# Optimization experiments

Hardware: AMD Instinct MI355X
Metric: run time of the kernel (lower is better)

The kernel has to match this reference:

```python
import jax, jax.numpy as jnp
import numpy as np

NN = 262144        # total nodes = 4096 graphs * 64 nodes
EN = 524288        # directed edges
IN_DIM = 32
H = 128
PROP_STEPS = 3


def setup_inputs() -> dict:
    key = jax.random.key(0)
    ks = jax.random.split(key, 16)
    s = lambda d: 1.0 / np.sqrt(d)
    x = jax.random.normal(ks[0], (NN, IN_DIM), dtype=jnp.float32)
    # edges: random within each 64-node graph block would be most faithful; random
    # over NN is the same access pattern workload-wise. Use per-graph-local edges.
    src = jax.random.randint(ks[1], (EN,), 0, NN, dtype=jnp.int64)
    dst = jax.random.randint(ks[2], (EN,), 0, NN, dtype=jnp.int64)
    edge_index = jnp.stack([src, dst], axis=0)
    return {
        "x": x,
        "edge_index": edge_index,
        "W_in": jax.random.normal(ks[3], (IN_DIM, H), jnp.float32) * s(IN_DIM),
        "b_in": jnp.zeros((H,), jnp.float32),
        "W_e1": jax.random.normal(ks[4], (H, H), jnp.float32) * s(H),
        "b_e1": jnp.zeros((H,), jnp.float32),
        "W_e2": jax.random.normal(ks[5], (H, H), jnp.float32) * s(H),
        "b_e2": jnp.zeros((H,), jnp.float32),
        "W_ih": jax.random.normal(ks[6], (H, 3 * H), jnp.float32) * s(H),
        "b_ih": jnp.zeros((3 * H,), jnp.float32),
        "W_hh": jax.random.normal(ks[7], (H, 3 * H), jnp.float32) * s(H),
        "b_hh": jnp.zeros((3 * H,), jnp.float32),
        "W_out": jax.random.normal(ks[8], (H, 1), jnp.float32) * s(H),
        "b_out": jnp.zeros((1,), jnp.float32),
    }


def reference(x, edge_index, W_in, b_in, W_e1, b_e1, W_e2, b_e2,
              W_ih, b_ih, W_hh, b_hh, W_out, b_out):
    in_node, out_node = edge_index[0], edge_index[1]
    nn = x.shape[0]
    # input MLP: Linear + tanh
    h = jnp.tanh(x @ W_in + b_in)                         # [NN, H]
    for _ in range(PROP_STEPS):
        # unified edge MLP (hidden tanh + linear out), applied per node then gathered
        m = jnp.tanh(h @ W_e1 + b_e1) @ W_e2 + b_e2       # [NN, H]
        msg = m[in_node]                                  # [EN, H] gather
        ssum = jax.ops.segment_sum(msg, out_node, num_segments=nn)
        cnt = jax.ops.segment_sum(jnp.ones((msg.shape[0],), msg.dtype),
                                  out_node, num_segments=nn)
        m_agg = ssum / jnp.maximum(cnt, 1.0)[:, None]     # scatter_mean, [NN, H]
        # GRU cell update: input = m_agg, hidden = h (torch GRUCell math)
        gi = m_agg @ W_ih + b_ih                          # [NN, 3H]
        gh = h @ W_hh + b_hh                              # [NN, 3H]
        i_r, i_z, i_n = jnp.split(gi, 3, axis=-1)
        h_r, h_z, h_n = jnp.split(gh, 3, axis=-1)
        r = jax.nn.sigmoid(i_r + h_r)
        z = jax.nn.sigmoid(i_z + h_z)
        n = jnp.tanh(i_n + r * h_n)
        h = (1.0 - z) * n + z * h
    # unified output head: single Linear
    return h @ W_out + b_out                              # [NN, 1]
```

## Files before the change

### kernel.cpp

```cpp
#include <hip/hip_runtime.h>

#define NN 262144
#define EN 524288
#define HD 128
#define IND 32

#define NT64  (NN/64)
#define GRID_E 768
#define NJOB  (NT64*2)
#define GRID_G2 512

typedef __attribute__((ext_vector_type(8))) short s16x8;
typedef __attribute__((ext_vector_type(4))) float f32x4;
typedef unsigned short u16;
typedef unsigned int u32;

#define MFMA(a,b,c) __builtin_amdgcn_mfma_f32_16x16x32_bf16(a,b,c,0,0,0)
#define SWZ(p) ((p) ^ ((((p)>>8)&7)<<4))

typedef __attribute__((address_space(1))) void gas_void;
typedef __attribute__((address_space(3))) void las_void;
__device__ __forceinline__ void gload16(const void* g, void* l){
  __builtin_amdgcn_global_load_lds((gas_void*)g, (las_void*)l, 16, 0, 0);
}

__device__ __forceinline__ u16 f2b(float f){
  u32 u = __builtin_bit_cast(u32, f);
  u = (u + 0x7fffu + ((u >> 16) & 1u)) >> 16;
  return (u16)u;
}
__device__ __forceinline__ u32 cvtpk(float lo, float hi){
  return (u32)f2b(lo) | ((u32)f2b(hi) << 16);
}
__device__ __forceinline__ float b2f(u32 lo16){ return __builtin_bit_cast(float, lo16 << 16); }
__device__ __forceinline__ float rcpf_(float x){ return __builtin_amdgcn_rcpf(x); }
__device__ __forceinline__ float exp2_(float x){ return __builtin_amdgcn_exp2f(x); }
__device__ __forceinline__ float fsig(float x){ return rcpf_(1.f + exp2_(x * -1.442695041f)); }
__device__ __forceinline__ float ftanh(float x){ return fmaf(-2.f, rcpf_(1.f + exp2_(x * 2.885390082f)), 1.f); }

__global__ __launch_bounds__(256) void k_w2bt(const float* __restrict__ W, u16* __restrict__ Wt, int K, int N){
  int idx = blockIdx.x*256 + threadIdx.x;
  if (idx >= K*N) return;
  int n = idx / K, k = idx - n*K;
  Wt[idx] = f2b(W[k*N + n]);
}

__global__ void k_eflag(const int* __restrict__ ei, int* __restrict__ flag){
  int v = ei[threadIdx.x*2 + 1];
  unsigned long long b = __ballot(v != 0);
  if (threadIdx.x == 0) flag[0] = (b == 0ULL) ? 1 : 0;
}
__device__ __forceinline__ int eget(const int* ei, int f, int which, int e){
  return f ? ei[(which*EN + e)*2] : ei[which*EN + e];
}

__global__ __launch_bounds__(256) void k_count(const int* __restrict__ ei, const int* __restrict__ flag, int* __restrict__ cnt){
  int e = blockIdx.x*256 + threadIdx.x;
  if (e < EN) atomicAdd(&cnt[eget(ei, flag[0], 1, e)], 1);
}
__global__ __launch_bounds__(256) void k_scan1(const int* __restrict__ cnt, int* __restrict__ excl, int* __restrict__ bsum){
  __shared__ int ws[4];
  int i = blockIdx.x*256 + threadIdx.x;
  int v = cnt[i];
  int ln = threadIdx.x & 63;
  int x = v;
  #pragma unroll
  for (int d=1; d<64; d<<=1){ int y = __shfl_up(x, d); if (ln >= d) x += y; }
  if (ln == 63) ws[threadIdx.x>>6] = x;
  __syncthreads();
  int wpre = 0;
  for (int j=0; j<(threadIdx.x>>6); ++j) wpre += ws[j];
  excl[i] = wpre + x - v;
  if (threadIdx.x == 255) bsum[blockIdx.x] = wpre + x;
}
__global__ __launch_bounds__(1024) void k_scan2(int* __restrict__ bsum){
  __shared__ int ws[16];
  int i = threadIdx.x;
  int v = bsum[i];
  int ln = i & 63;
  int x = v;
  #pragma unroll
  for (int d=1; d<64; d<<=1){ int y = __shfl_up(x, d); if (ln >= d) x += y; }
  if (ln == 63) ws[i>>6] = x;
  __syncthreads();
  int wpre = 0;
  for (int j=0; j<(i>>6); ++j) wpre += ws[j];
  bsum[i] = wpre + x - v;
}
__global__ __launch_bounds__(256) void k_scan3(const int* __restrict__ excl, const int* __restrict__ bsum, int* __restrict__ rp, int* __restrict__ cur){
  int i = blockIdx.x*256 + threadIdx.x;
  int v = excl[i] + bsum[blockIdx.x];
  rp[i] = v; cur[i] = v;
  if (i == 0) rp[NN] = EN;
}
__global__ __launch_bounds__(256) void k_fill(const int* __restrict__ ei, const int* __restrict__ flag, int* __restrict__ cur, int* __restrict__ cx){
  int e = blockIdx.x*256 + threadIdx.x;
  if (e >= EN) return;
  int f = flag[0];
  int p = atomicAdd(&cur[eget(ei, f, 1, e)], 1);
  cx[p] = eget(ei, f, 0, e);
}

__global__ __launch_bounds__(256) void k_input(const float* __restrict__ x, const u16* __restrict__ wt, const float* __restrict__ bias, u16* __restrict__ h){
  const int wv = threadIdx.x >> 6, ln = threadIdx.x & 63;
  const int l15 = ln & 15, lg = ln >> 4;
  const int base = blockIdx.x*128 + wv*32;
  s16x8 a[2];
  #pragma unroll
  for (int rt=0; rt<2; ++rt){
    const float* xp = x + (base + rt*16 + l15)*IND + lg*8;
    float4 v0 = *reinterpret_cast<const float4*>(xp);
    float4 v1 = *reinterpret_cast<const float4*>(xp + 4);
    s16x8 t;
    t[0]=(short)f2b(v0.x); t[1]=(short)f2b(v0.y); t[2]=(short)f2b(v0.z); t[3]=(short)f2b(v0.w);
    t[4]=(short)f2b(v1.x); t[5]=(short)f2b(v1.y); t[6]=(short)f2b(v1.z); t[7]=(short)f2b(v1.w);
    a[rt] = t;
  }
  #pragma unroll
  for (int cg=0; cg<8; ++cg){
    const int col = cg*16 + l15;
    s16x8 bf = *reinterpret_cast<const s16x8*>(wt + col*IND + lg*8);
    float bb = bias[col];
    f32x4 acc0 = {bb,bb,bb,bb}, acc1 = {bb,bb,bb,bb};
    acc0 = MFMA(a[0], bf, acc0);
    acc1 = MFMA(a[1], bf, acc1);
    #pragma unroll
    for (int r=0; r<4; ++r){
      h[(size_t)(base + lg*4 + r)*HD + col]      = f2b(ftanh(acc0[r]));
      h[(size_t)(base + 16 + lg*4 + r)*HD + col] = f2b(ftanh(acc1[r]));
    }
  }
}

__global__ __launch_bounds__(512) void k_edge(const u16* __restrict__ h, const u16* __restrict__ wt1, const float* __restrict__ b1,
                                              const u16* __restrict__ wt2, const float* __restrict__ b2, u16* __restrict__ m){
  extern __shared__ __align__(1024) unsigned char lds[];
  const int tid = threadIdx.x, wv = tid >> 6, ln = tid & 63;
  const int l15 = ln & 15, lg = ln >> 4;
  const int col = wv*16 + l15;

  s16x8 B1[4], B2[4];
  #pragma unroll
  for (int kk=0; kk<4; ++kk){
    const int ko = kk*32 + lg*8;
    B1[kk] = *reinterpret_cast<const s16x8*>(wt1 + (size_t)col*HD + ko);
    B2[kk] = *reinterpret_cast<const s16x8*>(wt2 + (size_t)col*HD + ko);
  }
  const float b1s = b1[col], b2s = b2[col];

  {
    const unsigned char* hg = (const unsigned char*)h + (size_t)blockIdx.x*64*256;
    #pragma unroll
    for (int i=0; i<2; ++i){
      int c = wv*2 + i;
      int p = c*1024 + ln*16;
      gload16(hg + SWZ(p), lds + c*1024);
    }
  }
  __syncthreads();

  unsigned char* tl = lds + 32768;
  int t = 0;
  #pragma unroll 1
  for (int tt = blockIdx.x; tt < NT64; tt += GRID_E, ++t){
    if (tt + GRID_E < NT64){
      const unsigned char* hg = (const unsigned char*)h + (size_t)(tt+GRID_E)*64*256;
      unsigned char* dst = lds + ((t+1)&1)*16384;
      #pragma unroll
      for (int i=0; i<2; ++i){
        int c = wv*2 + i;
        int p = c*1024 + ln*16;
        gload16(hg + SWZ(p), dst + c*1024);
      }
    }
    const unsigned char* hl = lds + (t&1)*16384;
    for (int rt=0; rt<4; ++rt){
      s16x8 a[4];
      #pragma unroll
      for (int kk=0; kk<4; ++kk){
        int row = rt*16 + l15;
        int p = row*256 + (((kk*4+lg) ^ (row&7))<<4);
        a[kk] = *reinterpret_cast<const s16x8*>(hl + p);
      }
      f32x4 acc = {b1s,b1s,b1s,b1s};
      __builtin_amdgcn_s_setprio(1);
      #pragma unroll
      for (int kk=0; kk<4; ++kk) acc = MFMA(a[kk], B1[kk], acc);
      __builtin_amdgcn_s_setprio(0);
      #pragma unroll
      for (int r=0; r<4; ++r){
        int row = rt*16 + lg*4 + r;
        int tb = row*256 + ((((col*2)>>4) ^ (row&7))<<4) + ((col&7)*2);
        *reinterpret_cast<u16*>(tl + tb) = f2b(ftanh(acc[r]));
      }
    }
    __syncthreads();
    for (int rt=0; rt<4; ++rt){
      s16x8 a[4];
      #pragma unroll
      for (int kk=0; kk<4; ++kk){
        int row = rt*16 + l15;
        int p = row*256 + (((kk*4+lg) ^ (row&7))<<4);
        a[kk] = *reinterpret_cast<const s16x8*>(tl + p);
      }
      f32x4 acc = {b2s,b2s,b2s,b2s};
      __builtin_amdgcn_s_setprio(1);
      #pragma unroll
      for (int kk=0; kk<4; ++kk) acc = MFMA(a[kk], B2[kk], acc);
      __builtin_amdgcn_s_setprio(0);
      u16* mp = m + (size_t)(tt*64 + rt*16 + lg*4)*HD + col;
      mp[0]    = f2b(acc[0]);
      mp[HD]   = f2b(acc[1]);
      mp[2*HD] = f2b(acc[2]);
      mp[3*HD] = f2b(acc[3]);
    }
    __syncthreads();
  }
}

__global__ __launch_bounds__(256) void k_agg(const u16* __restrict__ m, const int* __restrict__ rp, const int* __restrict__ cx, u16* __restrict__ magg){
  const int sub = threadIdx.x >> 5, l32 = threadIdx.x & 31;
  const int n = blockIdx.x*8 + sub;
  int s0 = rp[n], s1 = rp[n+1];
  float a0=0.f, a1=0.f, a2=0.f, a3=0.f;
  int p = s0;
  for (; p + 2 <= s1; p += 2){
    int na = cx[p], nb = cx[p+1];
    uint2 va = *reinterpret_cast<const uint2*>(m + (size_t)na*HD + l32*4);
    uint2 vb = *reinterpret_cast<const uint2*>(m + (size_t)nb*HD + l32*4);
    a0 += b2f(va.x & 0xffffu) + b2f(vb.x & 0xffffu);
    a1 += b2f(va.x >> 16)     + b2f(vb.x >> 16);
    a2 += b2f(va.y & 0xffffu) + b2f(vb.y & 0xffffu);
    a3 += b2f(va.y >> 16)     + b2f(vb.y >> 16);
  }
  if (p < s1){
    int na = cx[p];
    uint2 va = *reinterpret_cast<const uint2*>(m + (size_t)na*HD + l32*4);
    a0 += b2f(va.x & 0xffffu); a1 += b2f(va.x >> 16);
    a2 += b2f(va.y & 0xffffu); a3 += b2f(va.y >> 16);
  }
  int deg = s1 - s0;
  float inv = rcpf_((float)(deg > 0 ? deg : 1));
  uint2 o;
  o.x = cvtpk(a0*inv, a1*inv);
  o.y = cvtpk(a2*inv, a3*inv);
  *reinterpret_cast<uint2*>(magg + (size_t)n*HD + l32*4) = o;
}

__global__ __launch_bounds__(256, 2) void k_gru(const u16* __restrict__ magg, const u16* __restrict__ hin, u16* __restrict__ hout,
    const u16* __restrict__ wtih, const float* __restrict__ bih,
    const u16* __restrict__ wthh, const float* __restrict__ bhh){
  extern __shared__ __align__(1024) unsigned char lds[];
  const int tid = threadIdx.x, wv = tid >> 6, ln = tid & 63;
  const int l15 = ln & 15, lg = ln >> 4;
  const int ch = blockIdx.x & 1;
  const int col = ch*64 + wv*16 + l15;
  const int ce = col & ~1;

  s16x8 B[6][4];
  #pragma unroll
  for (int kk=0; kk<4; ++kk){
    const int ko = kk*32 + lg*8;
    B[0][kk] = *reinterpret_cast<const s16x8*>(wtih + (size_t)(col       )*HD + ko);
    B[1][kk] = *reinterpret_cast<const s16x8*>(wtih + (size_t)(col +   HD)*HD + ko);
    B[2][kk] = *reinterpret_cast<const s16x8*>(wtih + (size_t)(col + 2*HD)*HD + ko);
    B[3][kk] = *reinterpret_cast<const s16x8*>(wthh + (size_t)(col       )*HD + ko);
    B[4][kk] = *reinterpret_cast<const s16x8*>(wthh + (size_t)(col +   HD)*HD + ko);
    B[5][kk] = *reinterpret_cast<const s16x8*>(wthh + (size_t)(col + 2*HD)*HD + ko);
  }
  const float brz = bih[col] + bhh[col];
  const float bzz = bih[col+HD] + bhh[col+HD];
  const float bin_ = bih[col+2*HD], bhn_ = bhh[col+2*HD];

  {
    const size_t rbase = (size_t)(blockIdx.x >> 1)*64*256;
    const unsigned char* mg = (const unsigned char*)magg + rbase;
    const unsigned char* hg = (const unsigned char*)hin  + rbase;
    #pragma unroll
    for (int i=0; i<8; ++i){
      int c = wv*8 + i;
      int p = (c & 15)*1024 + ln*16;
      gload16((c < 16 ? mg : hg) + SWZ(p), lds + c*1024);
    }
  }
  __syncthreads();

#define LOADA(rt, amg, ahh, hld) { \
    const int row_ = (rt)*16 + l15; \
    _Pragma("unroll") \
    for (int kk=0; kk<4; ++kk){ \
      int p_ = row_*256 + (((kk*4+lg) ^ (row_&7))<<4); \
      amg[kk] = *reinterpret_cast<const s16x8*>(mgl + p_); \
      ahh[kk] = *reinterpret_cast<const s16x8*>(hl + p_); } \
    _Pragma("unroll") \
    for (int r_=0; r_<4; ++r_){ \
      int hrow_ = (rt)*16 + lg*4 + r_; \
      int hb_ = hrow_*256 + ((((ce*2)>>4) ^ (hrow_&7))<<4) + ((ce&7)*2); \
      hld[r_] = *reinterpret_cast<const u32*>(hl + hb_); } }

#define MFMAS(amg, ahh, aR, aZ, aN, aH) { \
    aR = (f32x4){brz,brz,brz,brz}; aZ = (f32x4){bzz,bzz,bzz,bzz}; \
    aN = (f32x4){bin_,bin_,bin_,bin_}; aH = (f32x4){bhn_,bhn_,bhn_,bhn_}; \
    __builtin_amdgcn_s_setprio(1); \
    _Pragma("unroll") \
    for (int kk=0; kk<4; ++kk){ \
      aR = MFMA(amg[kk], B[0][kk], aR); \
      aZ = MFMA(amg[kk], B[1][kk], aZ); \
      aN = MFMA(amg[kk], B[2][kk], aN); \
      aH = MFMA(ahh[kk], B[5][kk], aH); \
      aR = MFMA(ahh[kk], B[3][kk], aR); \
      aZ = MFMA(ahh[kk], B[4][kk], aZ); } \
    __builtin_amdgcn_s_setprio(0); }

#define EPI(rt, aR, aZ, aN, aH, hld) { \
    u16* hp_ = hout + (size_t)(rowt*64 + (rt)*16 + lg*4)*HD + col; \
    _Pragma("unroll") \
    for (int r_=0; r_<4; ++r_){ \
      float hold_ = __builtin_bit_cast(float, (col&1) ? (hld[r_] & 0xffff0000u) : (hld[r_] << 16)); \
      float rg_ = fsig(aR[r_]); \
      float zg_ = fsig(aZ[r_]); \
      float ng_ = ftanh(aN[r_] + rg_*aH[r_]); \
      hp_[r_*HD] = f2b(ng_ + zg_*(hold_ - ng_)); } }

  int t = 0;
  #pragma unroll 1
  for (int job = blockIdx.x; job < NJOB; job += GRID_G2, ++t){
    const int rowt = job >> 1;
    if (job + GRID_G2 < NJOB){
      const size_t rbase = (size_t)((job + GRID_G2) >> 1)*64*256;
      const unsigned char* mg = (const unsigned char*)magg + rbase;
      const unsigned char* hg = (const unsigned char*)hin  + rbase;
      unsigned char* dst = lds + ((t+1)&1)*32768;
      #pragma unroll
      for (int i=0; i<8; ++i){
        int c = wv*8 + i;
        int p = (c & 15)*1024 + ln*16;
        gload16((c < 16 ? mg : hg) + SWZ(p), dst + c*1024);
      }
    }
    const unsigned char* mgl = lds + (t&1)*32768;
    const unsigned char* hl  = mgl + 16384;

    s16x8 amgA[4], ahhA[4], amgB[4], ahhB[4];
    u32 hldA[4], hldB[4];
    f32x4 rA, zA, nA, hA, rB, zB, nB, hB;

    LOADA(0, amgA, ahhA, hldA); MFMAS(amgA, ahhA, rA, zA, nA, hA);
    LOADA(1, amgB, ahhB, hldB); MFMAS(amgB, ahhB, rB, zB, nB, hB); EPI(0, rA, zA, nA, hA, hldA);
    LOADA(2, amgA, ahhA, hldA); MFMAS(amgA, ahhA, rA, zA, nA, hA); EPI(1, rB, zB, nB, hB, hldB);
    LOADA(3, amgB, ahhB, hldB); MFMAS(amgB, ahhB, rB, zB, nB, hB); EPI(2, rA, zA, nA, hA, hldA);
    EPI(3, rB, zB, nB, hB, hldB);

    __syncthreads();
  }
#undef LOADA
#undef MFMAS
#undef EPI
}

__global__ __launch_bounds__(256) void k_out(const u16* __restrict__ h, const float* __restrict__ wo, const float* __restrict__ bo, float* __restrict__ out){
  const int wv = threadIdx.x >> 6, ln = threadIdx.x & 63;
  const int n = (blockIdx.x*4 + wv)*4 + (ln >> 4);
  const int kc = (ln & 15)*8;
  uint4 v = *reinterpret_cast<const uint4*>(h + (size_t)n*HD + kc);
  float4 w0 = *reinterpret_cast<const float4*>(wo + kc);
  float4 w1 = *reinterpret_cast<const float4*>(wo + kc + 4);
  float s = b2f(v.x & 0xffffu)*w0.x + b2f(v.x >> 16)*w0.y + b2f(v.y & 0xffffu)*w0.z + b2f(v.y >> 16)*w0.w
          + b2f(v.z & 0xffffu)*w1.x + b2f(v.z >> 16)*w1.y + b2f(v.w & 0xffffu)*w1.z + b2f(v.w >> 16)*w1.w;
  #pragma unroll
  for (int d=1; d<16; d<<=1) s += __shfl_xor(s, d, 16);
  if ((ln & 15) == 0) out[n] = s + bo[0];
}

#define AL256(x) ((((size_t)(x)) + 255) & ~(size_t)255)
static const size_t SZ_STATE = (size_t)NN*HD*2;
static const size_t OFF_HA   = 0;
static const size_t OFF_HB   = OFF_HA + SZ_STATE;
static const size_t OFF_MAGG = OFF_HB + SZ_STATE;
static const size_t OFF_RP   = OFF_MAGG + SZ_STATE;
static const size_t OFF_CUR  = OFF_RP + AL256((size_t)(NN+1)*4);
static const size_t OFF_CNT  = OFF_CUR + (size_t)NN*4;
static const size_t OFF_EXCL = OFF_CNT + (size_t)NN*4;
static const size_t OFF_BSUM = OFF_EXCL + (size_t)NN*4;
static const size_t OFF_CX   = OFF_BSUM + AL256(1024*4);
static const size_t OFF_FLAG = OFF_CX + (size_t)EN*4;
static const size_t OFF_WTIN = OFF_FLAG + 256;
static const size_t OFF_WTE1 = OFF_WTIN + AL256((size_t)IND*HD*2);
static const size_t OFF_WTE2 = OFF_WTE1 + AL256((size_t)HD*HD*2);
static const size_t OFF_WTIH = OFF_WTE2 + AL256((size_t)HD*HD*2);
static const size_t OFF_WTHH = OFF_WTIH + AL256((size_t)HD*3*HD*2);

extern "C" void kernel_launch(void* const* d_in, const int* in_sizes, int n_in,
                              void* d_out, int out_size, void* d_ws, size_t ws_size,
                              hipStream_t stream){
  const float* x    = (const float*)d_in[0];
  const int*   ei   = (const int*)d_in[1];
  const float* W_in = (const float*)d_in[2];  const float* b_in = (const float*)d_in[3];
  const float* W_e1 = (const float*)d_in[4];  const float* b_e1 = (const float*)d_in[5];
  const float* W_e2 = (const float*)d_in[6];  const float* b_e2 = (const float*)d_in[7];
  const float* W_ih = (const float*)d_in[8];  const float* b_ih = (const float*)d_in[9];
  const float* W_hh = (const float*)d_in[10]; const float* b_hh = (const float*)d_in[11];
  const float* W_out= (const float*)d_in[12]; const float* b_out= (const float*)d_in[13];
  float* out = (float*)d_out;

  char* ws = (char*)d_ws;
  u16* hA   = (u16*)(ws + OFF_HA);
  u16* hB   = (u16*)(ws + OFF_HB);
  u16* magg = (u16*)(ws + OFF_MAGG);
  int* rp   = (int*)(ws + OFF_RP);
  int* cur  = (int*)(ws + OFF_CUR);
  int* cnt  = (int*)(ws + OFF_CNT);
  int* excl = (int*)(ws + OFF_EXCL);
  int* bsum = (int*)(ws + OFF_BSUM);
  int* cx   = (int*)(ws + OFF_CX);
  int* flag = (int*)(ws + OFF_FLAG);
  u16* wtin = (u16*)(ws + OFF_WTIN);
  u16* wte1 = (u16*)(ws + OFF_WTE1);
  u16* wte2 = (u16*)(ws + OFF_WTE2);
  u16* wtih = (u16*)(ws + OFF_WTIH);
  u16* wthh = (u16*)(ws + OFF_WTHH);

  hipFuncSetAttribute((const void*)k_edge, hipFuncAttributeMaxDynamicSharedMemorySize, 49152);
  hipFuncSetAttribute((const void*)k_gru,  hipFuncAttributeMaxDynamicSharedMemorySize, 65536);

  hipMemsetAsync(cnt, 0, (size_t)NN*4, stream);

  k_w2bt<<<(IND*HD + 255)/256, 256, 0, stream>>>(W_in, wtin, IND, HD);
  k_w2bt<<<(HD*HD + 255)/256, 256, 0, stream>>>(W_e1, wte1, HD, HD);
  k_w2bt<<<(HD*HD + 255)/256, 256, 0, stream>>>(W_e2, wte2, HD, HD);
  k_w2bt<<<(HD*3*HD + 255)/256, 256, 0, stream>>>(W_ih, wtih, HD, 3*HD);
  k_w2bt<<<(HD*3*HD + 255)/256, 256, 0, stream>>>(W_hh, wthh, HD, 3*HD);

  k_eflag<<<1, 64, 0, stream>>>(ei, flag);
  k_count<<<EN/256, 256, 0, stream>>>(ei, flag, cnt);
  k_scan1<<<NN/256, 256, 0, stream>>>(cnt, excl, bsum);
  k_scan2<<<1, 1024, 0, stream>>>(bsum);
  k_scan3<<<NN/256, 256, 0, stream>>>(excl, bsum, rp, cur);
  k_fill<<<EN/256, 256, 0, stream>>>(ei, flag, cur, cx);

  k_input<<<NN/128, 256, 0, stream>>>(x, wtin, b_in, hA);

  for (int it=0; it<3; ++it){
    u16* hin  = (it & 1) ? hB : hA;
    u16* hout = (it & 1) ? hA : hB;
    k_edge<<<GRID_E, 512, 49152, stream>>>(hin, wte1, b_e1, wte2, b_e2, hout);
    k_agg<<<NN/8, 256, 0, stream>>>(hout, rp, cx, magg);
    k_gru<<<GRID_G2, 256, 65536, stream>>>(magg, hin, hout, wtih, b_ih, wthh, b_hh);
  }
  k_out<<<NN/16, 256, 0, stream>>>(hB, W_out, b_out, out);
}
```

Baseline: 527.3 us.

## Fuse neighbor mean aggregation into GRU kernel, drop separate k_agg pass

Removes the standalone aggregation kernel. The GRU kernel now gathers neighbor messages via CSR for its 64-row tile, averages them in registers and writes the result straight into swizzled LDS, so the magg buffer no longer makes a round trip through global memory. The edge kernel writes messages to a dedicated buffer instead of hout. Only h is prefetched double-buffered, LDS drops to 48KB and the grid grows to 768. The trade-off is that the irregular gather now runs serially inside the GRU blocks, one edge at a time with 8 threads per row, and is not overlapped with the MFMA work.

```diff
diff --git a/kernel.cpp b/kernel.cpp
--- a/kernel.cpp
+++ b/kernel.cpp
@@ -8,7 +8,7 @@
 #define NT64  (NN/64)
 #define GRID_E 768
 #define NJOB  (NT64*2)
-#define GRID_G2 512
+#define GRID_G 768
 
 typedef __attribute__((ext_vector_type(8))) short s16x8;
 typedef __attribute__((ext_vector_type(4))) float f32x4;
@@ -218,36 +218,8 @@
   }
 }
 
-__global__ __launch_bounds__(256) void k_agg(const u16* __restrict__ m, const int* __restrict__ rp, const int* __restrict__ cx, u16* __restrict__ magg){
-  const int sub = threadIdx.x >> 5, l32 = threadIdx.x & 31;
-  const int n = blockIdx.x*8 + sub;
-  int s0 = rp[n], s1 = rp[n+1];
-  float a0=0.f, a1=0.f, a2=0.f, a3=0.f;
-  int p = s0;
-  for (; p + 2 <= s1; p += 2){
-    int na = cx[p], nb = cx[p+1];
-    uint2 va = *reinterpret_cast<const uint2*>(m + (size_t)na*HD + l32*4);
-    uint2 vb = *reinterpret_cast<const uint2*>(m + (size_t)nb*HD + l32*4);
-    a0 += b2f(va.x & 0xffffu) + b2f(vb.x & 0xffffu);
-    a1 += b2f(va.x >> 16)     + b2f(vb.x >> 16);
-    a2 += b2f(va.y & 0xffffu) + b2f(vb.y & 0xffffu);
-    a3 += b2f(va.y >> 16)     + b2f(vb.y >> 16);
-  }
-  if (p < s1){
-    int na = cx[p];
-    uint2 va = *reinterpret_cast<const uint2*>(m + (size_t)na*HD + l32*4);
-    a0 += b2f(va.x & 0xffffu); a1 += b2f(va.x >> 16);
-    a2 += b2f(va.y & 0xffffu); a3 += b2f(va.y >> 16);
-  }
-  int deg = s1 - s0;
-  float inv = rcpf_((float)(deg > 0 ? deg : 1));
-  uint2 o;
-  o.x = cvtpk(a0*inv, a1*inv);
-  o.y = cvtpk(a2*inv, a3*inv);
-  *reinterpret_cast<uint2*>(magg + (size_t)n*HD + l32*4) = o;
-}
-
-__global__ __launch_bounds__(256, 2) void k_gru(const u16* __restrict__ magg, const u16* __restrict__ hin, u16* __restrict__ hout,
+__global__ __launch_bounds__(256, 2) void k_gru(const u16* __restrict__ mbuf, const int* __restrict__ rp, const int* __restrict__ cx,
+    const u16* __restrict__ hin, u16* __restrict__ hout,
     const u16* __restrict__ wtih, const float* __restrict__ bih,
     const u16* __restrict__ wthh, const float* __restrict__ bhh){
   extern __shared__ __align__(1024) unsigned char lds[];
@@ -273,17 +245,16 @@
   const float bin_ = bih[col+2*HD], bhn_ = bhh[col+2*HD];
 
   {
-    const size_t rbase = (size_t)(blockIdx.x >> 1)*64*256;
-    const unsigned char* mg = (const unsigned char*)magg + rbase;
-    const unsigned char* hg = (const unsigned char*)hin  + rbase;
+    const unsigned char* hg = (const unsigned char*)hin + (size_t)(blockIdx.x >> 1)*64*256;
     #pragma unroll
-    for (int i=0; i<8; ++i){
-      int c = wv*8 + i;
-      int p = (c & 15)*1024 + ln*16;
-      gload16((c < 16 ? mg : hg) + SWZ(p), lds + c*1024);
-    }
-  }
-  __syncthreads();
+    for (int i=0; i<4; ++i){
+      int c = wv*4 + i;
+      int p = c*1024 + ln*16;
+      gload16(hg + SWZ(p), lds + 16384 + c*1024);
+    }
+  }
+
+  const int gr = tid >> 3, gc = tid & 7;
 
 #define LOADA(rt, amg, ahh, hld) { \
     const int row_ = (rt)*16 + l15; \
@@ -324,22 +295,58 @@
 
   int t = 0;
   #pragma unroll 1
-  for (int job = blockIdx.x; job < NJOB; job += GRID_G2, ++t){
+  for (int job = blockIdx.x; job < NJOB; job += GRID_G, ++t){
     const int rowt = job >> 1;
-    if (job + GRID_G2 < NJOB){
-      const size_t rbase = (size_t)((job + GRID_G2) >> 1)*64*256;
-      const unsigned char* mg = (const unsigned char*)magg + rbase;
-      const unsigned char* hg = (const unsigned char*)hin  + rbase;
-      unsigned char* dst = lds + ((t+1)&1)*32768;
-      #pragma unroll
-      for (int i=0; i<8; ++i){
-        int c = wv*8 + i;
-        int p = (c & 15)*1024 + ln*16;
-        gload16((c < 16 ? mg : hg) + SWZ(p), dst + c*1024);
-      }
-    }
-    const unsigned char* mgl = lds + (t&1)*32768;
-    const unsigned char* hl  = mgl + 16384;
+
+    #pragma unroll 1
+    for (int pp=0; pp<2; ++pp){
+      int r = pp*32 + gr;
+      int n = rowt*64 + r;
+      int s0 = rp[n], s1 = rp[n+1];
+      float a[16];
+      #pragma unroll
+      for (int j=0; j<16; ++j) a[j] = 0.f;
+      #pragma unroll 1
+      for (int e = s0; e < s1; ++e){
+        int src = cx[e];
+        const u16* mr = mbuf + (size_t)src*HD + gc*16;
+        uint4 v0 = *reinterpret_cast<const uint4*>(mr);
+        uint4 v1 = *reinterpret_cast<const uint4*>(mr + 8);
+        a[0]  += b2f(v0.x & 0xffffu); a[1]  += b2f(v0.x >> 16);
+        a[2]  += b2f(v0.y & 0xffffu); a[3]  += b2f(v0.y >> 16);
+        a[4]  += b2f(v0.z & 0xffffu); a[5]  += b2f(v0.z >> 16);
+        a[6]  += b2f(v0.w & 0xffffu); a[7]  += b2f(v0.w >> 16);
+        a[8]  += b2f(v1.x & 0xffffu); a[9]  += b2f(v1.x >> 16);
+        a[10] += b2f(v1.y & 0xffffu); a[11] += b2f(v1.y >> 16);
+        a[12] += b2f(v1.z & 0xffffu); a[13] += b2f(v1.z >> 16);
+        a[14] += b2f(v1.w & 0xffffu); a[15] += b2f(v1.w >> 16);
+      }
+      int deg = s1 - s0;
+      float inv = rcpf_((float)(deg > 0 ? deg : 1));
+      uint4 w0, w1;
+      w0.x = cvtpk(a[0]*inv,  a[1]*inv);  w0.y = cvtpk(a[2]*inv,  a[3]*inv);
+      w0.z = cvtpk(a[4]*inv,  a[5]*inv);  w0.w = cvtpk(a[6]*inv,  a[7]*inv);
+      w1.x = cvtpk(a[8]*inv,  a[9]*inv);  w1.y = cvtpk(a[10]*inv, a[11]*inv);
+      w1.z = cvtpk(a[12]*inv, a[13]*inv); w1.w = cvtpk(a[14]*inv, a[15]*inv);
+      int g0 = r*256 + gc*32;
+      *reinterpret_cast<uint4*>(lds + SWZ(g0))      = w0;
+      *reinterpret_cast<uint4*>(lds + SWZ(g0 + 16)) = w1;
+    }
+    __syncthreads();
+
+    if (job + GRID_G < NJOB){
+      const unsigned char* hg = (const unsigned char*)hin + (size_t)((job + GRID_G) >> 1)*64*256;
+      unsigned char* dst = lds + 16384 + ((t+1)&1)*16384;
+      #pragma unroll
+      for (int i=0; i<4; ++i){
+        int c = wv*4 + i;
+        int p = c*1024 + ln*16;
+        gload16(hg + SWZ(p), dst + c*1024);
+      }
+    }
+
+    const unsigned char* mgl = lds;
+    const unsigned char* hl  = lds + 16384 + (t&1)*16384;
 
     s16x8 amgA[4], ahhA[4], amgB[4], ahhB[4];
     u32 hldA[4], hldB[4];
@@ -376,8 +383,8 @@
 static const size_t SZ_STATE = (size_t)NN*HD*2;
 static const size_t OFF_HA   = 0;
 static const size_t OFF_HB   = OFF_HA + SZ_STATE;
-static const size_t OFF_MAGG = OFF_HB + SZ_STATE;
-static const size_t OFF_RP   = OFF_MAGG + SZ_STATE;
+static const size_t OFF_M    = OFF_HB + SZ_STATE;
+static const size_t OFF_RP   = OFF_M + SZ_STATE;
 static const size_t OFF_CUR  = OFF_RP + AL256((size_t)(NN+1)*4);
 static const size_t OFF_CNT  = OFF_CUR + (size_t)NN*4;
 static const size_t OFF_EXCL = OFF_CNT + (size_t)NN*4;
@@ -406,7 +413,7 @@
   char* ws = (char*)d_ws;
   u16* hA   = (u16*)(ws + OFF_HA);
   u16* hB   = (u16*)(ws + OFF_HB);
-  u16* magg = (u16*)(ws + OFF_MAGG);
+  u16* mbuf = (u16*)(ws + OFF_M);
   int* rp   = (int*)(ws + OFF_RP);
   int* cur  = (int*)(ws + OFF_CUR);
   int* cnt  = (int*)(ws + OFF_CNT);
@@ -421,7 +428,7 @@
   u16* wthh = (u16*)(ws + OFF_WTHH);
 
   hipFuncSetAttribute((const void*)k_edge, hipFuncAttributeMaxDynamicSharedMemorySize, 49152);
-  hipFuncSetAttribute((const void*)k_gru,  hipFuncAttributeMaxDynamicSharedMemorySize, 65536);
+  hipFuncSetAttribute((const void*)k_gru,  hipFuncAttributeMaxDynamicSharedMemorySize, 49152);
 
   hipMemsetAsync(cnt, 0, (size_t)NN*4, stream);
 
@@ -443,9 +450,8 @@
   for (int it=0; it<3; ++it){
     u16* hin  = (it & 1) ? hB : hA;
     u16* hout = (it & 1) ? hA : hB;
-    k_edge<<<GRID_E, 512, 49152, stream>>>(hin, wte1, b_e1, wte2, b_e2, hout);
-    k_agg<<<NN/8, 256, 0, stream>>>(hout, rp, cx, magg);
-    k_gru<<<GRID_G2, 256, 65536, stream>>>(magg, hin, hout, wtih, b_ih, wthh, b_hh);
+    k_edge<<<GRID_E, 512, 49152, stream>>>(hin, wte1, b_e1, wte2, b_e2, mbuf);
+    k_gru<<<GRID_G, 256, 49152, stream>>>(mbuf, rp, cx, hin, hout, wtih, b_ih, wthh, b_hh);
   }
   k_out<<<NN/16, 256, 0, stream>>>(hB, W_out, b_out, out);
 }
```

Result: slower. 850.0 us (+61.2%).

## Drop GRU double buffering, double grid, and remap blocks for XCD locality

Applied to the files above, without the earlier changes.

The GRU kernel stops double-buffering its magg/h row tiles in LDS. It now loads one 32KB tile, synchronises, then computes, which halves its LDS use and lets launch bounds allow 4 blocks per CU with 1024 blocks. The block-to-tile mapping is changed so that the two column-half blocks of a row tile share an XCD (blockIdx mod 8) and can reuse the tile in L2. The cost is that global loads no longer overlap compute within a block and must be hidden by the higher occupancy instead. Register pressure under the 4-blocks bound may also cause spills, given the 24 preloaded B fragments.

```diff
diff --git a/kernel.cpp b/kernel.cpp
--- a/kernel.cpp
+++ b/kernel.cpp
@@ -7,8 +7,7 @@
 
 #define NT64  (NN/64)
 #define GRID_E 768
-#define NJOB  (NT64*2)
-#define GRID_G2 512
+#define GRID_G 1024
 
 typedef __attribute__((ext_vector_type(8))) short s16x8;
 typedef __attribute__((ext_vector_type(4))) float f32x4;
@@ -247,13 +246,16 @@
   *reinterpret_cast<uint2*>(magg + (size_t)n*HD + l32*4) = o;
 }
 
-__global__ __launch_bounds__(256, 2) void k_gru(const u16* __restrict__ magg, const u16* __restrict__ hin, u16* __restrict__ hout,
+__global__ __launch_bounds__(256, 4) void k_gru(const u16* __restrict__ magg, const u16* __restrict__ hin, u16* __restrict__ hout,
     const u16* __restrict__ wtih, const float* __restrict__ bih,
     const u16* __restrict__ wthh, const float* __restrict__ bhh){
   extern __shared__ __align__(1024) unsigned char lds[];
   const int tid = threadIdx.x, wv = tid >> 6, ln = tid & 63;
   const int l15 = ln & 15, lg = ln >> 4;
-  const int ch = blockIdx.x & 1;
+  const int xcd = blockIdx.x & 7;
+  const int q   = blockIdx.x >> 3;
+  const int ch  = q & 1;
+  const int p0  = (q >> 1)*8 + xcd;
   const int col = ch*64 + wv*16 + l15;
   const int ce = col & ~1;
 
@@ -271,19 +273,6 @@
   const float brz = bih[col] + bhh[col];
   const float bzz = bih[col+HD] + bhh[col+HD];
   const float bin_ = bih[col+2*HD], bhn_ = bhh[col+2*HD];
-
-  {
-    const size_t rbase = (size_t)(blockIdx.x >> 1)*64*256;
-    const unsigned char* mg = (const unsigned char*)magg + rbase;
-    const unsigned char* hg = (const unsigned char*)hin  + rbase;
-    #pragma unroll
-    for (int i=0; i<8; ++i){
-      int c = wv*8 + i;
-      int p = (c & 15)*1024 + ln*16;
-      gload16((c < 16 ? mg : hg) + SWZ(p), lds + c*1024);
-    }
-  }
-  __syncthreads();
 
 #define LOADA(rt, amg, ahh, hld) { \
     const int row_ = (rt)*16 + l15; \
@@ -322,24 +311,23 @@
       float ng_ = ftanh(aN[r_] + rg_*aH[r_]); \
       hp_[r_*HD] = f2b(ng_ + zg_*(hold_ - ng_)); } }
 
-  int t = 0;
   #pragma unroll 1
-  for (int job = blockIdx.x; job < NJOB; job += GRID_G2, ++t){
-    const int rowt = job >> 1;
-    if (job + GRID_G2 < NJOB){
-      const size_t rbase = (size_t)((job + GRID_G2) >> 1)*64*256;
+  for (int rowt = p0; rowt < NT64; rowt += 512){
+    {
+      const size_t rbase = (size_t)rowt*64*256;
       const unsigned char* mg = (const unsigned char*)magg + rbase;
       const unsigned char* hg = (const unsigned char*)hin  + rbase;
-      unsigned char* dst = lds + ((t+1)&1)*32768;
       #pragma unroll
       for (int i=0; i<8; ++i){
         int c = wv*8 + i;
         int p = (c & 15)*1024 + ln*16;
-        gload16((c < 16 ? mg : hg) + SWZ(p), dst + c*1024);
+        gload16((c < 16 ? mg : hg) + SWZ(p), lds + c*1024);
       }
     }
-    const unsigned char* mgl = lds + (t&1)*32768;
-    const unsigned char* hl  = mgl + 16384;
+    __syncthreads();
+
+    const unsigned char* mgl = lds;
+    const unsigned char* hl  = lds + 16384;
 
     s16x8 amgA[4], ahhA[4], amgB[4], ahhB[4];
     u32 hldA[4], hldB[4];
@@ -421,7 +409,7 @@
   u16* wthh = (u16*)(ws + OFF_WTHH);
 
   hipFuncSetAttribute((const void*)k_edge, hipFuncAttributeMaxDynamicSharedMemorySize, 49152);
-  hipFuncSetAttribute((const void*)k_gru,  hipFuncAttributeMaxDynamicSharedMemorySize, 65536);
+  hipFuncSetAttribute((const void*)k_gru,  hipFuncAttributeMaxDynamicSharedMemorySize, 32768);
 
   hipMemsetAsync(cnt, 0, (size_t)NN*4, stream);
 
@@ -445,7 +433,7 @@
     u16* hout = (it & 1) ? hA : hB;
     k_edge<<<GRID_E, 512, 49152, stream>>>(hin, wte1, b_e1, wte2, b_e2, hout);
     k_agg<<<NN/8, 256, 0, stream>>>(hout, rp, cx, magg);
-    k_gru<<<GRID_G2, 256, 65536, stream>>>(magg, hin, hout, wtih, b_ih, wthh, b_hh);
+    k_gru<<<GRID_G, 256, 32768, stream>>>(magg, hin, hout, wtih, b_ih, wthh, b_hh);
   }
   k_out<<<NN/16, 256, 0, stream>>>(hB, W_out, b_out, out);
 }
```

After: 1.676 ms. 218% more time.
